# Kernel tuning notes

Measured on AMD Instinct MI355X. Metric: run time of the kernel, lower is better.

## Reference

```python
import jax, jax.numpy as jnp
import numpy as np

B, S, D = 1, 2048, 2048
H, KVH, HD = 32, 8, 64  # heads, kv heads, head_dim
GROUPS = H // KVH
SCALE = HD ** -0.5


def rotate_half(x):
    x1, x2 = jnp.split(x, 2, axis=-1)
    return jnp.concatenate((-x2, x1), axis=-1)


def setup_inputs() -> dict:
    key = jax.random.key(0)
    ks = jax.random.split(key, 8)
    hidden_states = jax.random.normal(ks[0], (B, S, D), dtype=jnp.float32)
    # RoPE tables: [B, S, HD]
    inv_freq = 1.0 / (10000.0 ** (jnp.arange(0, HD, 2, dtype=jnp.float32) / HD))
    t = jnp.arange(S, dtype=jnp.float32)
    freqs = jnp.outer(t, inv_freq)                      # [S, HD/2]
    emb = jnp.concatenate((freqs, freqs), axis=-1)      # [S, HD]
    cos = jnp.cos(emb)[None]                            # [1, S, HD]
    sin = jnp.sin(emb)[None]
    std = 0.02
    wq = jax.random.normal(ks[1], (H * HD, D), dtype=jnp.float32) * std
    wk = jax.random.normal(ks[2], (KVH * HD, D), dtype=jnp.float32) * std
    wv = jax.random.normal(ks[3], (KVH * HD, D), dtype=jnp.float32) * std
    wo = jax.random.normal(ks[4], (D, H * HD), dtype=jnp.float32) * std
    return {"hidden_states": hidden_states, "cos": cos, "sin": sin,
            "wq": wq, "wk": wk, "wv": wv, "wo": wo}


def reference(hidden_states, cos, sin, wq, wk, wv, wo):
    b, s, d = hidden_states.shape
    # QKV projections (nn.Linear: x @ W.T), split into heads -> [B, H, S, HD]
    q = (hidden_states @ wq.T).reshape(b, s, H, HD).transpose(0, 2, 1, 3)
    k = (hidden_states @ wk.T).reshape(b, s, KVH, HD).transpose(0, 2, 1, 3)
    v = (hidden_states @ wv.T).reshape(b, s, KVH, HD).transpose(0, 2, 1, 3)
    # RoPE (unsqueeze_dim=1)
    c = cos[:, None, :, :]
    sn = sin[:, None, :, :]
    q = q * c + rotate_half(q) * sn
    k = k * c + rotate_half(k) * sn
    # GQA: repeat kv heads to match query heads
    k = jnp.repeat(k, GROUPS, axis=1)
    v = jnp.repeat(v, GROUPS, axis=1)
    # scaled causal softmax attention
    scores = jnp.einsum('bhqd,bhkd->bhqk', q, k) * SCALE
    causal = jnp.tril(jnp.ones((s, s), dtype=bool))
    scores = jnp.where(causal, scores, jnp.finfo(scores.dtype).min)
    probs = jax.nn.softmax(scores, axis=-1)
    attn = jnp.einsum('bhqk,bhkd->bhqd', probs, v)
    attn = attn.transpose(0, 2, 1, 3).reshape(b, s, H * HD)
    return attn @ wo.T
```

## Files before the change

### kernel.cpp

```cpp
#include <hip/hip_runtime.h>
#include <stdint.h>

#define SEQ   2048
#define DMODEL 2048
#define NQH   32
#define NKVH  8
#define HDIM  64
#define QN    (NQH*HDIM)
#define KVNN  (NKVH*HDIM)

typedef __bf16 bf16x8 __attribute__((ext_vector_type(8)));
typedef float  f32x4  __attribute__((ext_vector_type(4)));
typedef unsigned short u16;

__device__ __forceinline__ u16 f2bf(float f) {
  uint32_t u = __builtin_bit_cast(uint32_t, f);
  u += 0x7fffu + ((u >> 16) & 1u);
  return (u16)(u >> 16);
}
__device__ __forceinline__ float bf2f(u16 b) {
  return __builtin_bit_cast(float, (uint32_t)b << 16);
}
__device__ __forceinline__ bool probe_is_f32(const uint32_t* p) {
  return (p[0] & 0xFFFFu) == 0u;
}

__device__ __forceinline__ void glds16(const u16* g, void* lds) {
  __builtin_amdgcn_global_load_lds(
      (const __attribute__((address_space(1))) uint32_t*)g,
      (__attribute__((address_space(3))) uint32_t*)lds, 16, 0, 0);
}

__global__ __launch_bounds__(256)
void conv_all(const void* __restrict__ X, const void* __restrict__ cosv,
              const void* __restrict__ sinv, const void* __restrict__ wq,
              const void* __restrict__ wk, const void* __restrict__ wv,
              const void* __restrict__ wo,
              u16* __restrict__ Xc, u16* __restrict__ cosc, u16* __restrict__ sinc,
              u16* __restrict__ wqc, u16* __restrict__ wkc, u16* __restrict__ wvc,
              u16* __restrict__ woc)
{
  const bool f32in = probe_is_f32((const uint32_t*)cosv);
  const long t = (long)blockIdx.x * 256 + threadIdx.x;
  const void* src; u16* dst; long off;
  if      (t < 524288L)  { src = X;    dst = Xc;   off = t; }
  else if (t < 1048576L) { src = wq;   dst = wqc;  off = t - 524288L; }
  else if (t < 1179648L) { src = wk;   dst = wkc;  off = t - 1048576L; }
  else if (t < 1310720L) { src = wv;   dst = wvc;  off = t - 1179648L; }
  else if (t < 1835008L) { src = wo;   dst = woc;  off = t - 1310720L; }
  else if (t < 1851392L) { src = cosv; dst = cosc; off = t - 1835008L; }
  else                   { src = sinv; dst = sinc; off = t - 1851392L; }
  if (f32in) {
    const float4* s = (const float4*)src;
    float4 a = s[2*off], b = s[2*off + 1];
    union { u16 h[8]; uint4 u; } o;
    o.h[0]=f2bf(a.x); o.h[1]=f2bf(a.y); o.h[2]=f2bf(a.z); o.h[3]=f2bf(a.w);
    o.h[4]=f2bf(b.x); o.h[5]=f2bf(b.y); o.h[6]=f2bf(b.z); o.h[7]=f2bf(b.w);
    *(uint4*)(dst + off*8) = o.u;
  } else {
    *(uint4*)(dst + off*8) = ((const uint4*)src)[off];
  }
}

__global__ __launch_bounds__(256, 4)
void gemm_qkv(const u16* __restrict__ A,
              const u16* __restrict__ wq, const u16* __restrict__ wk,
              const u16* __restrict__ wv,
              u16* __restrict__ Qb, u16* __restrict__ Kb, u16* __restrict__ Vb)
{
  __shared__ __align__(16) u16 As[64][32];
  __shared__ __align__(16) u16 Bs[128][32];
  const int tid  = threadIdx.x;
  const int wave = tid >> 6;
  const int lane = tid & 63;
  const int quad = lane >> 4;
  const int l16  = lane & 15;
  const int m0 = blockIdx.y * 64;
  const int n0 = blockIdx.x * 128;
  const int wm = (wave & 1) * 32;
  const int wn = (wave >> 1) * 64;
  const int K = DMODEL;
  const int lr = lane >> 2;
  const int lc = (lane & 3) * 8;

  const u16* Bbase; u16* Cbase; int Cstride, nc0;
  if (n0 < 2048)      { Bbase = wq + (size_t)n0 * K;          Cbase = Qb; Cstride = QN;   nc0 = n0; }
  else if (n0 < 2560) { Bbase = wk + (size_t)(n0 - 2048) * K; Cbase = Kb; Cstride = KVNN; nc0 = n0 - 2048; }
  else                { Bbase = wv + (size_t)(n0 - 2560) * K; Cbase = Vb; Cstride = KVNN; nc0 = n0 - 2560; }

  f32x4 acc[2][4];
  #pragma unroll
  for (int i = 0; i < 2; i++)
    #pragma unroll
    for (int j = 0; j < 4; j++)
      acc[i][j] = (f32x4){0.f, 0.f, 0.f, 0.f};

  for (int k0 = 0; k0 < K; k0 += 32) {
    __syncthreads();
    glds16(A + (size_t)(m0 + 16*wave + lr) * K + k0 + lc,
           (char*)&As[0][0] + wave*1024);
    glds16(Bbase + (size_t)(16*wave + lr) * K + k0 + lc,
           (char*)&Bs[0][0] + wave*1024);
    glds16(Bbase + (size_t)(64 + 16*wave + lr) * K + k0 + lc,
           (char*)&Bs[0][0] + (4+wave)*1024);
    __syncthreads();
    bf16x8 af[2], bfr[4];
    #pragma unroll
    for (int i = 0; i < 2; i++) af[i]  = *(const bf16x8*)&As[wm + i*16 + l16][quad*8];
    #pragma unroll
    for (int j = 0; j < 4; j++) bfr[j] = *(const bf16x8*)&Bs[wn + j*16 + l16][quad*8];
    #pragma unroll
    for (int i = 0; i < 2; i++)
      #pragma unroll
      for (int j = 0; j < 4; j++)
        acc[i][j] = __builtin_amdgcn_mfma_f32_16x16x32_bf16(af[i], bfr[j], acc[i][j], 0, 0, 0);
  }

  #pragma unroll
  for (int i = 0; i < 2; i++) {
    const int rb = m0 + wm + i*16 + quad*4;
    #pragma unroll
    for (int j = 0; j < 4; j++) {
      const int col = nc0 + wn + j*16 + l16;
      #pragma unroll
      for (int r = 0; r < 4; r++)
        Cbase[(size_t)(rb + r) * Cstride + col] = f2bf(acc[i][j][r]);
    }
  }
}

__global__ __launch_bounds__(256, 4)
void gemm_nt(const u16* __restrict__ A, const u16* __restrict__ B,
             void* __restrict__ C, int M, int N, int K,
             const uint32_t* outprobe)
{
  __shared__ __align__(16) u16 As[64][32];
  __shared__ __align__(16) u16 Bs[128][32];
  const int tid  = threadIdx.x;
  const int wave = tid >> 6;
  const int lane = tid & 63;
  const int quad = lane >> 4;
  const int l16  = lane & 15;
  const int m0 = blockIdx.y * 64;
  const int n0 = blockIdx.x * 128;
  const int wm = (wave & 1) * 32;
  const int wn = (wave >> 1) * 64;
  const int lr = lane >> 2;
  const int lc = (lane & 3) * 8;

  f32x4 acc[2][4];
  #pragma unroll
  for (int i = 0; i < 2; i++)
    #pragma unroll
    for (int j = 0; j < 4; j++)
      acc[i][j] = (f32x4){0.f, 0.f, 0.f, 0.f};

  for (int k0 = 0; k0 < K; k0 += 32) {
    __syncthreads();
    glds16(A + (size_t)(m0 + 16*wave + lr) * K + k0 + lc,
           (char*)&As[0][0] + wave*1024);
    glds16(B + (size_t)(n0 + 16*wave + lr) * K + k0 + lc,
           (char*)&Bs[0][0] + wave*1024);
    glds16(B + (size_t)(n0 + 64 + 16*wave + lr) * K + k0 + lc,
           (char*)&Bs[0][0] + (4+wave)*1024);
    __syncthreads();
    bf16x8 af[2], bfr[4];
    #pragma unroll
    for (int i = 0; i < 2; i++) af[i]  = *(const bf16x8*)&As[wm + i*16 + l16][quad*8];
    #pragma unroll
    for (int j = 0; j < 4; j++) bfr[j] = *(const bf16x8*)&Bs[wn + j*16 + l16][quad*8];
    #pragma unroll
    for (int i = 0; i < 2; i++)
      #pragma unroll
      for (int j = 0; j < 4; j++)
        acc[i][j] = __builtin_amdgcn_mfma_f32_16x16x32_bf16(af[i], bfr[j], acc[i][j], 0, 0, 0);
  }

  const bool f32out = (outprobe != nullptr) && probe_is_f32(outprobe);
  #pragma unroll
  for (int i = 0; i < 2; i++) {
    const int rb = m0 + wm + i*16 + quad*4;
    #pragma unroll
    for (int j = 0; j < 4; j++) {
      const int col = n0 + wn + j*16 + l16;
      if (f32out) {
        float* Cf = (float*)C;
        #pragma unroll
        for (int r = 0; r < 4; r++)
          Cf[(size_t)(rb + r) * N + col] = acc[i][j][r];
      } else {
        u16* Ch = (u16*)C;
        #pragma unroll
        for (int r = 0; r < 4; r++)
          Ch[(size_t)(rb + r) * N + col] = f2bf(acc[i][j][r]);
      }
    }
  }
}

__global__ void rope_k(u16* __restrict__ Kb,
                       const u16* __restrict__ cosb, const u16* __restrict__ sinb)
{
  const int idx = blockIdx.x * 256 + threadIdx.x;
  const int s = idx >> 8;
  const int rem = idx & 255;
  u16* base = Kb + (size_t)s * KVNN + (rem >> 5) * 64;
  const int d = rem & 31;
  const float x1 = bf2f(base[d]);
  const float x2 = bf2f(base[d + 32]);
  const float c  = bf2f(cosb[s * 64 + d]);
  const float sn = bf2f(sinb[s * 64 + d]);
  base[d]      = f2bf(x1 * c - x2 * sn);
  base[d + 32] = f2bf(x2 * c + x1 * sn);
}

__global__ __launch_bounds__(256)
void vtrans(const u16* __restrict__ Vb, u16* __restrict__ Vtg)
{
  __shared__ __align__(16) u16 T[64][72];
  const int tid = threadIdx.x;
  const int hkv = blockIdx.x & 7;
  const int s0  = (blockIdx.x >> 3) * 64;
  const int r = tid >> 3;
  const int c = (tid & 7) * 8;
  *(uint4*)&T[r][c]      = *(const uint4*)(Vb + (size_t)(s0 + r)      * KVNN + hkv*64 + c);
  *(uint4*)&T[r + 32][c] = *(const uint4*)(Vb + (size_t)(s0 + r + 32) * KVNN + hkv*64 + c);
  __syncthreads();
  #pragma unroll
  for (int dd = 0; dd < 64; dd += 32) {
    const int d = (tid >> 3) + dd;
    union { u16 h[8]; uint4 u; } o;
    #pragma unroll
    for (int j = 0; j < 8; j++) o.h[j] = T[c + j][d];
    *(uint4*)(Vtg + (size_t)(hkv*64 + d) * SEQ + s0 + c) = o.u;
  }
}

__device__ __forceinline__ float qmax16(float v) {
  v = fmaxf(v, __shfl_xor(v, 1)); v = fmaxf(v, __shfl_xor(v, 2));
  v = fmaxf(v, __shfl_xor(v, 4)); v = fmaxf(v, __shfl_xor(v, 8));
  return v;
}
__device__ __forceinline__ float qsum16(float v) {
  v += __shfl_xor(v, 1); v += __shfl_xor(v, 2);
  v += __shfl_xor(v, 4); v += __shfl_xor(v, 8);
  return v;
}

__global__ __launch_bounds__(256, 4)
void attn_kernel(const u16* __restrict__ Qb,
                 const u16* __restrict__ Kb,
                 const u16* __restrict__ Vtg,
                 u16* __restrict__ Ob,
                 const u16* __restrict__ cosb, const u16* __restrict__ sinb)
{
  __shared__ __align__(16) u16 Ks[64][72];
  __shared__ __align__(16) u16 Vt[64][72];
  __shared__ __align__(16) u16 Ps[4][16][72];

  const int tid  = threadIdx.x;
  const int wave = tid >> 6;
  const int lane = tid & 63;
  const int quad = lane >> 4;
  const int l16  = lane & 15;
  const int h    = blockIdx.x;
  const int qt   = 31 - blockIdx.y;
  const int hkv  = h >> 2;
  const int qrow0 = qt * 64 + wave * 16;
  const int ktmax = qt + 1;

  bf16x8 qf[2];
  {
    const int qrow = qrow0 + l16;
    const u16* qp = Qb + (size_t)qrow * QN + h*64 + quad*8;
    union { bf16x8 v; u16 h8[8]; } lo, hi, cv, sv, olo, ohi;
    lo.v = *(const bf16x8*)qp;
    hi.v = *(const bf16x8*)(qp + 32);
    cv.v = *(const bf16x8*)(cosb + qrow*64 + quad*8);
    sv.v = *(const bf16x8*)(sinb + qrow*64 + quad*8);
    #pragma unroll
    for (int j = 0; j < 8; j++) {
      const float x1 = bf2f(lo.h8[j]), x2 = bf2f(hi.h8[j]);
      const float c = bf2f(cv.h8[j]), sn = bf2f(sv.h8[j]);
      olo.h8[j] = f2bf((x1*c - x2*sn) * 0.125f);
      ohi.h8[j] = f2bf((x2*c + x1*sn) * 0.125f);
    }
    qf[0] = olo.v;
    qf[1] = ohi.v;
  }

  f32x4 oacc[4];
  #pragma unroll
  for (int nt = 0; nt < 4; nt++) oacc[nt] = (f32x4){0.f, 0.f, 0.f, 0.f};
  float m_run[4], l_run[4];
  #pragma unroll
  for (int r = 0; r < 4; r++) { m_run[r] = -1e30f; l_run[r] = 0.f; }

  const int sr = tid >> 3;
  const int sc = (tid & 7) * 8;

  uint4 k0, k1, v0, v1;
  {
    k0 = *(const uint4*)(Kb + (size_t)(sr)      * KVNN + hkv*64 + sc);
    k1 = *(const uint4*)(Kb + (size_t)(sr + 32) * KVNN + hkv*64 + sc);
    v0 = *(const uint4*)(Vtg + (size_t)(hkv*64 + sr)      * SEQ + sc);
    v1 = *(const uint4*)(Vtg + (size_t)(hkv*64 + sr + 32) * SEQ + sc);
  }

  for (int kt = 0; kt < ktmax; kt++) {
    const int kb = kt * 64;
    const bool diag = (kt == qt);

    __syncthreads();
    *(uint4*)&Ks[sr][sc]      = k0;
    *(uint4*)&Ks[sr + 32][sc] = k1;
    *(uint4*)&Vt[sr][sc]      = v0;
    *(uint4*)&Vt[sr + 32][sc] = v1;
    __syncthreads();

    if (kt + 1 < ktmax) {
      const int kn = kb + 64;
      k0 = *(const uint4*)(Kb + (size_t)(kn + sr)      * KVNN + hkv*64 + sc);
      k1 = *(const uint4*)(Kb + (size_t)(kn + sr + 32) * KVNN + hkv*64 + sc);
      v0 = *(const uint4*)(Vtg + (size_t)(hkv*64 + sr)      * SEQ + kn + sc);
      v1 = *(const uint4*)(Vtg + (size_t)(hkv*64 + sr + 32) * SEQ + kn + sc);
    }

    f32x4 sacc[4];
    #pragma unroll
    for (int nt = 0; nt < 4; nt++) sacc[nt] = (f32x4){0.f, 0.f, 0.f, 0.f};
    #pragma unroll
    for (int ks = 0; ks < 2; ks++)
      #pragma unroll
      for (int nt = 0; nt < 4; nt++)
        if (!diag || nt <= wave) {
          bf16x8 kf = *(const bf16x8*)&Ks[nt*16 + l16][ks*32 + quad*8];
          sacc[nt] = __builtin_amdgcn_mfma_f32_16x16x32_bf16(qf[ks], kf, sacc[nt], 0, 0, 0);
        }
    if (diag) {
      #pragma unroll
      for (int nt = 0; nt < 4; nt++)
        #pragma unroll
        for (int r = 0; r < 4; r++)
          if (kb + nt*16 + l16 > qrow0 + quad*4 + r)
            sacc[nt][r] = -1e30f;
    }
    float alpha[4];
    #pragma unroll
    for (int r = 0; r < 4; r++) {
      float mx = fmaxf(fmaxf(sacc[0][r], sacc[1][r]), fmaxf(sacc[2][r], sacc[3][r]));
      mx = qmax16(mx);
      const float mnew = fmaxf(m_run[r], mx);
      alpha[r] = __expf(m_run[r] - mnew);
      m_run[r] = mnew;
      float rs = 0.f;
      #pragma unroll
      for (int nt = 0; nt < 4; nt++) {
        const float p = __expf(sacc[nt][r] - mnew);
        rs += p;
        Ps[wave][quad*4 + r][nt*16 + l16] = f2bf(p);
      }
      rs = qsum16(rs);
      l_run[r] = l_run[r] * alpha[r] + rs;
    }
    #pragma unroll
    for (int nt = 0; nt < 4; nt++)
      #pragma unroll
      for (int r = 0; r < 4; r++)
        oacc[nt][r] *= alpha[r];
    asm volatile("" ::: "memory");
    #pragma unroll
    for (int ks = 0; ks < 2; ks++) {
      if (diag && wave < 2 && ks == 1) continue;
      bf16x8 pf = *(const bf16x8*)&Ps[wave][l16][ks*32 + quad*8];
      #pragma unroll
      for (int nt = 0; nt < 4; nt++) {
        bf16x8 vf = *(const bf16x8*)&Vt[nt*16 + l16][ks*32 + quad*8];
        oacc[nt] = __builtin_amdgcn_mfma_f32_16x16x32_bf16(pf, vf, oacc[nt], 0, 0, 0);
      }
    }
  }

  #pragma unroll
  for (int r = 0; r < 4; r++) {
    const float inv = 1.0f / l_run[r];
    const int qrow = qrow0 + quad*4 + r;
    #pragma unroll
    for (int nt = 0; nt < 4; nt++)
      Ob[(size_t)qrow * QN + h*64 + nt*16 + l16] = f2bf(oacc[nt][r] * inv);
  }
}

extern "C" void kernel_launch(void* const* d_in, const int* in_sizes, int n_in,
                              void* d_out, int out_size, void* d_ws, size_t ws_size,
                              hipStream_t stream) {
  const void* X    = d_in[0];
  const void* cosr = d_in[1];
  const void* sinr = d_in[2];
  const void* wq   = d_in[3];
  const void* wk   = d_in[4];
  const void* wv   = d_in[5];
  const void* wo   = d_in[6];

  char* ws = (char*)d_ws;
  const size_t MB = 1024u * 1024u;
  u16* Xc   = (u16*)(ws);
  u16* wqc  = (u16*)(ws + 8*MB);
  u16* wkc  = (u16*)(ws + 16*MB);
  u16* wvc  = (u16*)(ws + 18*MB);
  u16* woc  = (u16*)(ws + 20*MB);
  u16* cosc = (u16*)(ws + 28*MB);
  u16* sinc = (u16*)(ws + 28*MB + 256*1024);
  u16* Qb   = (u16*)(ws + 28*MB + 512*1024);
  u16* Kb   = (u16*)(ws + 36*MB + 512*1024);
  u16* Vb   = (u16*)(ws + 38*MB + 512*1024);
  u16* Vtg  = (u16*)(ws + 40*MB + 512*1024);
  u16* Ab   = wqc;

  dim3 blk(256);
  conv_all<<<dim3(7296), blk, 0, stream>>>(X, cosr, sinr, wq, wk, wv, wo,
                                           Xc, cosc, sinc, wqc, wkc, wvc, woc);
  gemm_qkv<<<dim3(24, 32), blk, 0, stream>>>(Xc, wqc, wkc, wvc, Qb, Kb, Vb);
  rope_k<<<dim3((SEQ*NKVH*32)/256), blk, 0, stream>>>(Kb, cosc, sinc);
  vtrans<<<dim3(256), blk, 0, stream>>>(Vb, Vtg);
  attn_kernel<<<dim3(NQH, SEQ/64), blk, 0, stream>>>(Qb, Kb, Vtg, Ab, cosc, sinc);
  gemm_nt<<<dim3(16, 32), blk, 0, stream>>>(Ab, woc, d_out, SEQ, DMODEL, DMODEL,
                                            (const uint32_t*)cosr);
}
```

Baseline: 258.4 us.

## Double-buffer LDS and enlarge GEMM tiles to 128x128 in QKV and output projections

Both projection GEMMs move from 64x128 to 128x128 block tiles, so each wave computes a 64x64 sub-tile with 16 MFMAs per k-step instead of 8. The LDS staging becomes double-buffered: the next k-slice is prefetched with global_load_lds while the current one is consumed, leaving one barrier per iteration instead of two. This is meant to raise arithmetic intensity and hide global load latency. In exchange the grids halve to 384 and 256 blocks, occupancy drops to 2 blocks per CU, and register pressure rises, which may leave the 256-CU device underfilled.

```diff
diff --git a/kernel.cpp b/kernel.cpp
--- a/kernel.cpp
+++ b/kernel.cpp
@@ -29,6 +29,9 @@
   __builtin_amdgcn_global_load_lds(
       (const __attribute__((address_space(1))) uint32_t*)g,
       (__attribute__((address_space(3))) uint32_t*)lds, 16, 0, 0);
+}
+__device__ __forceinline__ void drain_vm() {
+  asm volatile("s_waitcnt vmcnt(0)" ::: "memory");
 }
 
 __global__ __launch_bounds__(256)
@@ -62,22 +65,22 @@
   }
 }
 
-__global__ __launch_bounds__(256, 4)
+__global__ __launch_bounds__(256, 2)
 void gemm_qkv(const u16* __restrict__ A,
               const u16* __restrict__ wq, const u16* __restrict__ wk,
               const u16* __restrict__ wv,
               u16* __restrict__ Qb, u16* __restrict__ Kb, u16* __restrict__ Vb)
 {
-  __shared__ __align__(16) u16 As[64][32];
-  __shared__ __align__(16) u16 Bs[128][32];
+  __shared__ __align__(16) u16 As[2][128][32];
+  __shared__ __align__(16) u16 Bs[2][128][32];
   const int tid  = threadIdx.x;
   const int wave = tid >> 6;
   const int lane = tid & 63;
   const int quad = lane >> 4;
   const int l16  = lane & 15;
-  const int m0 = blockIdx.y * 64;
+  const int m0 = blockIdx.y * 128;
   const int n0 = blockIdx.x * 128;
-  const int wm = (wave & 1) * 32;
+  const int wm = (wave & 1) * 64;
   const int wn = (wave >> 1) * 64;
   const int K = DMODEL;
   const int lr = lane >> 2;
@@ -88,36 +91,49 @@
   else if (n0 < 2560) { Bbase = wk + (size_t)(n0 - 2048) * K; Cbase = Kb; Cstride = KVNN; nc0 = n0 - 2048; }
   else                { Bbase = wv + (size_t)(n0 - 2560) * K; Cbase = Vb; Cstride = KVNN; nc0 = n0 - 2560; }
 
-  f32x4 acc[2][4];
-  #pragma unroll
-  for (int i = 0; i < 2; i++)
+  f32x4 acc[4][4];
+  #pragma unroll
+  for (int i = 0; i < 4; i++)
     #pragma unroll
     for (int j = 0; j < 4; j++)
       acc[i][j] = (f32x4){0.f, 0.f, 0.f, 0.f};
 
+  #define STAGE_QKV(b, k0)                                                        \
+    do {                                                                          \
+      glds16(A + (size_t)(m0 + 32*wave + lr) * K + (k0) + lc,                     \
+             (char*)&As[b][0][0] + wave*2048);                                    \
+      glds16(A + (size_t)(m0 + 32*wave + 16 + lr) * K + (k0) + lc,                \
+             (char*)&As[b][0][0] + wave*2048 + 1024);                             \
+      glds16(Bbase + (size_t)(32*wave + lr) * K + (k0) + lc,                      \
+             (char*)&Bs[b][0][0] + wave*2048);                                    \
+      glds16(Bbase + (size_t)(32*wave + 16 + lr) * K + (k0) + lc,                 \
+             (char*)&Bs[b][0][0] + wave*2048 + 1024);                             \
+    } while (0)
+
+  STAGE_QKV(0, 0);
+  drain_vm();
+  __syncthreads();
+  int cur = 0;
   for (int k0 = 0; k0 < K; k0 += 32) {
-    __syncthreads();
-    glds16(A + (size_t)(m0 + 16*wave + lr) * K + k0 + lc,
-           (char*)&As[0][0] + wave*1024);
-    glds16(Bbase + (size_t)(16*wave + lr) * K + k0 + lc,
-           (char*)&Bs[0][0] + wave*1024);
-    glds16(Bbase + (size_t)(64 + 16*wave + lr) * K + k0 + lc,
-           (char*)&Bs[0][0] + (4+wave)*1024);
-    __syncthreads();
-    bf16x8 af[2], bfr[4];
-    #pragma unroll
-    for (int i = 0; i < 2; i++) af[i]  = *(const bf16x8*)&As[wm + i*16 + l16][quad*8];
-    #pragma unroll
-    for (int j = 0; j < 4; j++) bfr[j] = *(const bf16x8*)&Bs[wn + j*16 + l16][quad*8];
-    #pragma unroll
-    for (int i = 0; i < 2; i++)
+    if (k0 + 32 < K) STAGE_QKV(cur ^ 1, k0 + 32);
+    bf16x8 af[4], bfr[4];
+    #pragma unroll
+    for (int i = 0; i < 4; i++) af[i]  = *(const bf16x8*)&As[cur][wm + i*16 + l16][quad*8];
+    #pragma unroll
+    for (int j = 0; j < 4; j++) bfr[j] = *(const bf16x8*)&Bs[cur][wn + j*16 + l16][quad*8];
+    #pragma unroll
+    for (int i = 0; i < 4; i++)
       #pragma unroll
       for (int j = 0; j < 4; j++)
         acc[i][j] = __builtin_amdgcn_mfma_f32_16x16x32_bf16(af[i], bfr[j], acc[i][j], 0, 0, 0);
-  }
-
-  #pragma unroll
-  for (int i = 0; i < 2; i++) {
+    drain_vm();
+    __syncthreads();
+    cur ^= 1;
+  }
+  #undef STAGE_QKV
+
+  #pragma unroll
+  for (int i = 0; i < 4; i++) {
     const int rb = m0 + wm + i*16 + quad*4;
     #pragma unroll
     for (int j = 0; j < 4; j++) {
@@ -129,56 +145,69 @@
   }
 }
 
-__global__ __launch_bounds__(256, 4)
+__global__ __launch_bounds__(256, 2)
 void gemm_nt(const u16* __restrict__ A, const u16* __restrict__ B,
              void* __restrict__ C, int M, int N, int K,
              const uint32_t* outprobe)
 {
-  __shared__ __align__(16) u16 As[64][32];
-  __shared__ __align__(16) u16 Bs[128][32];
+  __shared__ __align__(16) u16 As[2][128][32];
+  __shared__ __align__(16) u16 Bs[2][128][32];
   const int tid  = threadIdx.x;
   const int wave = tid >> 6;
   const int lane = tid & 63;
   const int quad = lane >> 4;
   const int l16  = lane & 15;
-  const int m0 = blockIdx.y * 64;
+  const int m0 = blockIdx.y * 128;
   const int n0 = blockIdx.x * 128;
-  const int wm = (wave & 1) * 32;
+  const int wm = (wave & 1) * 64;
   const int wn = (wave >> 1) * 64;
   const int lr = lane >> 2;
   const int lc = (lane & 3) * 8;
 
-  f32x4 acc[2][4];
-  #pragma unroll
-  for (int i = 0; i < 2; i++)
+  f32x4 acc[4][4];
+  #pragma unroll
+  for (int i = 0; i < 4; i++)
     #pragma unroll
     for (int j = 0; j < 4; j++)
       acc[i][j] = (f32x4){0.f, 0.f, 0.f, 0.f};
 
+  #define STAGE_NT(b, k0)                                                         \
+    do {                                                                          \
+      glds16(A + (size_t)(m0 + 32*wave + lr) * K + (k0) + lc,                     \
+             (char*)&As[b][0][0] + wave*2048);                                    \
+      glds16(A + (size_t)(m0 + 32*wave + 16 + lr) * K + (k0) + lc,                \
+             (char*)&As[b][0][0] + wave*2048 + 1024);                             \
+      glds16(B + (size_t)(n0 + 32*wave + lr) * K + (k0) + lc,                     \
+             (char*)&Bs[b][0][0] + wave*2048);                                    \
+      glds16(B + (size_t)(n0 + 32*wave + 16 + lr) * K + (k0) + lc,                \
+             (char*)&Bs[b][0][0] + wave*2048 + 1024);                             \
+    } while (0)
+
+  STAGE_NT(0, 0);
+  drain_vm();
+  __syncthreads();
+  int cur = 0;
   for (int k0 = 0; k0 < K; k0 += 32) {
-    __syncthreads();
-    glds16(A + (size_t)(m0 + 16*wave + lr) * K + k0 + lc,
-           (char*)&As[0][0] + wave*1024);
-    glds16(B + (size_t)(n0 + 16*wave + lr) * K + k0 + lc,
-           (char*)&Bs[0][0] + wave*1024);
-    glds16(B + (size_t)(n0 + 64 + 16*wave + lr) * K + k0 + lc,
-           (char*)&Bs[0][0] + (4+wave)*1024);
-    __syncthreads();
-    bf16x8 af[2], bfr[4];
-    #pragma unroll
-    for (int i = 0; i < 2; i++) af[i]  = *(const bf16x8*)&As[wm + i*16 + l16][quad*8];
-    #pragma unroll
-    for (int j = 0; j < 4; j++) bfr[j] = *(const bf16x8*)&Bs[wn + j*16 + l16][quad*8];
-    #pragma unroll
-    for (int i = 0; i < 2; i++)
+    if (k0 + 32 < K) STAGE_NT(cur ^ 1, k0 + 32);
+    bf16x8 af[4], bfr[4];
+    #pragma unroll
+    for (int i = 0; i < 4; i++) af[i]  = *(const bf16x8*)&As[cur][wm + i*16 + l16][quad*8];
+    #pragma unroll
+    for (int j = 0; j < 4; j++) bfr[j] = *(const bf16x8*)&Bs[cur][wn + j*16 + l16][quad*8];
+    #pragma unroll
+    for (int i = 0; i < 4; i++)
       #pragma unroll
       for (int j = 0; j < 4; j++)
         acc[i][j] = __builtin_amdgcn_mfma_f32_16x16x32_bf16(af[i], bfr[j], acc[i][j], 0, 0, 0);
-  }
+    drain_vm();
+    __syncthreads();
+    cur ^= 1;
+  }
+  #undef STAGE_NT
 
   const bool f32out = (outprobe != nullptr) && probe_is_f32(outprobe);
   #pragma unroll
-  for (int i = 0; i < 2; i++) {
+  for (int i = 0; i < 4; i++) {
     const int rb = m0 + wm + i*16 + quad*4;
     #pragma unroll
     for (int j = 0; j < 4; j++) {
@@ -420,10 +449,10 @@
   dim3 blk(256);
   conv_all<<<dim3(7296), blk, 0, stream>>>(X, cosr, sinr, wq, wk, wv, wo,
                                            Xc, cosc, sinc, wqc, wkc, wvc, woc);
-  gemm_qkv<<<dim3(24, 32), blk, 0, stream>>>(Xc, wqc, wkc, wvc, Qb, Kb, Vb);
+  gemm_qkv<<<dim3(24, 16), blk, 0, stream>>>(Xc, wqc, wkc, wvc, Qb, Kb, Vb);
   rope_k<<<dim3((SEQ*NKVH*32)/256), blk, 0, stream>>>(Kb, cosc, sinc);
   vtrans<<<dim3(256), blk, 0, stream>>>(Vb, Vtg);
   attn_kernel<<<dim3(NQH, SEQ/64), blk, 0, stream>>>(Qb, Kb, Vtg, Ab, cosc, sinc);
-  gemm_nt<<<dim3(16, 32), blk, 0, stream>>>(Ab, woc, d_out, SEQ, DMODEL, DMODEL,
+  gemm_nt<<<dim3(16, 16), blk, 0, stream>>>(Ab, woc, d_out, SEQ, DMODEL, DMODEL,
                                             (const uint32_t*)cosr);
 }
```

After: 268.3 us. 3.8% more time.

## Double-buffer GEMM LDS tiles, use native bf16 conversion and exp2 softmax

Applied to the files above, without the earlier changes.

Both GEMM kernels get double-buffered LDS tiles. Each step prefetches the next K-slice with global_load_lds while computing MFMA on the current one, with one barrier per iteration instead of two. The attention softmax now scales scores by log2(e) and uses a hardware exp2 builtin instead of __expf, and f2bf uses the compiler's native bf16 conversion. Doubling LDS may reduce occupancy, and the full vmcnt(0) drain each iteration limits how much overlap is achieved.

```diff
diff --git a/kernel.cpp b/kernel.cpp
--- a/kernel.cpp
+++ b/kernel.cpp
@@ -14,12 +14,18 @@
 typedef unsigned short u16;
 
 __device__ __forceinline__ u16 f2bf(float f) {
-  uint32_t u = __builtin_bit_cast(uint32_t, f);
-  u += 0x7fffu + ((u >> 16) & 1u);
-  return (u16)(u >> 16);
+  __bf16 h = (__bf16)f;
+  return __builtin_bit_cast(u16, h);
 }
 __device__ __forceinline__ float bf2f(u16 b) {
   return __builtin_bit_cast(float, (uint32_t)b << 16);
+}
+__device__ __forceinline__ float fexp2(float x) {
+#if __has_builtin(__builtin_amdgcn_exp2f)
+  return __builtin_amdgcn_exp2f(x);
+#else
+  return __expf(0.69314718056f * x);
+#endif
 }
 __device__ __forceinline__ bool probe_is_f32(const uint32_t* p) {
   return (p[0] & 0xFFFFu) == 0u;
@@ -29,6 +35,9 @@
   __builtin_amdgcn_global_load_lds(
       (const __attribute__((address_space(1))) uint32_t*)g,
       (__attribute__((address_space(3))) uint32_t*)lds, 16, 0, 0);
+}
+__device__ __forceinline__ void drain_vm() {
+  asm volatile("s_waitcnt vmcnt(0)" ::: "memory");
 }
 
 __global__ __launch_bounds__(256)
@@ -68,8 +77,8 @@
               const u16* __restrict__ wv,
               u16* __restrict__ Qb, u16* __restrict__ Kb, u16* __restrict__ Vb)
 {
-  __shared__ __align__(16) u16 As[64][32];
-  __shared__ __align__(16) u16 Bs[128][32];
+  __shared__ __align__(16) u16 As[2][64][32];
+  __shared__ __align__(16) u16 Bs[2][128][32];
   const int tid  = threadIdx.x;
   const int wave = tid >> 6;
   const int lane = tid & 63;
@@ -95,26 +104,37 @@
     for (int j = 0; j < 4; j++)
       acc[i][j] = (f32x4){0.f, 0.f, 0.f, 0.f};
 
+  #define STAGE_QKV(b, k0)                                                        \
+    do {                                                                          \
+      glds16(A + (size_t)(m0 + 16*wave + lr) * K + (k0) + lc,                     \
+             (char*)&As[b][0][0] + wave*1024);                                    \
+      glds16(Bbase + (size_t)(16*wave + lr) * K + (k0) + lc,                      \
+             (char*)&Bs[b][0][0] + wave*1024);                                    \
+      glds16(Bbase + (size_t)(64 + 16*wave + lr) * K + (k0) + lc,                 \
+             (char*)&Bs[b][0][0] + (4+wave)*1024);                                \
+    } while (0)
+
+  STAGE_QKV(0, 0);
+  drain_vm();
+  __syncthreads();
+  int cur = 0;
   for (int k0 = 0; k0 < K; k0 += 32) {
-    __syncthreads();
-    glds16(A + (size_t)(m0 + 16*wave + lr) * K + k0 + lc,
-           (char*)&As[0][0] + wave*1024);
-    glds16(Bbase + (size_t)(16*wave + lr) * K + k0 + lc,
-           (char*)&Bs[0][0] + wave*1024);
-    glds16(Bbase + (size_t)(64 + 16*wave + lr) * K + k0 + lc,
-           (char*)&Bs[0][0] + (4+wave)*1024);
-    __syncthreads();
+    if (k0 + 32 < K) STAGE_QKV(cur ^ 1, k0 + 32);
     bf16x8 af[2], bfr[4];
     #pragma unroll
-    for (int i = 0; i < 2; i++) af[i]  = *(const bf16x8*)&As[wm + i*16 + l16][quad*8];
-    #pragma unroll
-    for (int j = 0; j < 4; j++) bfr[j] = *(const bf16x8*)&Bs[wn + j*16 + l16][quad*8];
+    for (int i = 0; i < 2; i++) af[i]  = *(const bf16x8*)&As[cur][wm + i*16 + l16][quad*8];
+    #pragma unroll
+    for (int j = 0; j < 4; j++) bfr[j] = *(const bf16x8*)&Bs[cur][wn + j*16 + l16][quad*8];
     #pragma unroll
     for (int i = 0; i < 2; i++)
       #pragma unroll
       for (int j = 0; j < 4; j++)
         acc[i][j] = __builtin_amdgcn_mfma_f32_16x16x32_bf16(af[i], bfr[j], acc[i][j], 0, 0, 0);
-  }
+    drain_vm();
+    __syncthreads();
+    cur ^= 1;
+  }
+  #undef STAGE_QKV
 
   #pragma unroll
   for (int i = 0; i < 2; i++) {
@@ -134,8 +154,8 @@
              void* __restrict__ C, int M, int N, int K,
              const uint32_t* outprobe)
 {
-  __shared__ __align__(16) u16 As[64][32];
-  __shared__ __align__(16) u16 Bs[128][32];
+  __shared__ __align__(16) u16 As[2][64][32];
+  __shared__ __align__(16) u16 Bs[2][128][32];
   const int tid  = threadIdx.x;
   const int wave = tid >> 6;
   const int lane = tid & 63;
@@ -155,26 +175,37 @@
     for (int j = 0; j < 4; j++)
       acc[i][j] = (f32x4){0.f, 0.f, 0.f, 0.f};
 
+  #define STAGE_NT(b, k0)                                                         \
+    do {                                                                          \
+      glds16(A + (size_t)(m0 + 16*wave + lr) * K + (k0) + lc,                     \
+             (char*)&As[b][0][0] + wave*1024);                                    \
+      glds16(B + (size_t)(n0 + 16*wave + lr) * K + (k0) + lc,                     \
+             (char*)&Bs[b][0][0] + wave*1024);                                    \
+      glds16(B + (size_t)(n0 + 64 + 16*wave + lr) * K + (k0) + lc,                \
+             (char*)&Bs[b][0][0] + (4+wave)*1024);                                \
+    } while (0)
+
+  STAGE_NT(0, 0);
+  drain_vm();
+  __syncthreads();
+  int cur = 0;
   for (int k0 = 0; k0 < K; k0 += 32) {
-    __syncthreads();
-    glds16(A + (size_t)(m0 + 16*wave + lr) * K + k0 + lc,
-           (char*)&As[0][0] + wave*1024);
-    glds16(B + (size_t)(n0 + 16*wave + lr) * K + k0 + lc,
-           (char*)&Bs[0][0] + wave*1024);
-    glds16(B + (size_t)(n0 + 64 + 16*wave + lr) * K + k0 + lc,
-           (char*)&Bs[0][0] + (4+wave)*1024);
-    __syncthreads();
+    if (k0 + 32 < K) STAGE_NT(cur ^ 1, k0 + 32);
     bf16x8 af[2], bfr[4];
     #pragma unroll
-    for (int i = 0; i < 2; i++) af[i]  = *(const bf16x8*)&As[wm + i*16 + l16][quad*8];
-    #pragma unroll
-    for (int j = 0; j < 4; j++) bfr[j] = *(const bf16x8*)&Bs[wn + j*16 + l16][quad*8];
+    for (int i = 0; i < 2; i++) af[i]  = *(const bf16x8*)&As[cur][wm + i*16 + l16][quad*8];
+    #pragma unroll
+    for (int j = 0; j < 4; j++) bfr[j] = *(const bf16x8*)&Bs[cur][wn + j*16 + l16][quad*8];
     #pragma unroll
     for (int i = 0; i < 2; i++)
       #pragma unroll
       for (int j = 0; j < 4; j++)
         acc[i][j] = __builtin_amdgcn_mfma_f32_16x16x32_bf16(af[i], bfr[j], acc[i][j], 0, 0, 0);
-  }
+    drain_vm();
+    __syncthreads();
+    cur ^= 1;
+  }
+  #undef STAGE_NT
 
   const bool f32out = (outprobe != nullptr) && probe_is_f32(outprobe);
   #pragma unroll
@@ -236,6 +267,8 @@
   }
 }
 
+#define LOG2E 1.4426950408889634f
+
 __device__ __forceinline__ float qmax16(float v) {
   v = fmaxf(v, __shfl_xor(v, 1)); v = fmaxf(v, __shfl_xor(v, 2));
   v = fmaxf(v, __shfl_xor(v, 4)); v = fmaxf(v, __shfl_xor(v, 8));
@@ -337,6 +370,11 @@
           bf16x8 kf = *(const bf16x8*)&Ks[nt*16 + l16][ks*32 + quad*8];
           sacc[nt] = __builtin_amdgcn_mfma_f32_16x16x32_bf16(qf[ks], kf, sacc[nt], 0, 0, 0);
         }
+    #pragma unroll
+    for (int nt = 0; nt < 4; nt++)
+      #pragma unroll
+      for (int r = 0; r < 4; r++)
+        sacc[nt][r] *= LOG2E;
     if (diag) {
       #pragma unroll
       for (int nt = 0; nt < 4; nt++)
@@ -351,12 +389,12 @@
       float mx = fmaxf(fmaxf(sacc[0][r], sacc[1][r]), fmaxf(sacc[2][r], sacc[3][r]));
       mx = qmax16(mx);
       const float mnew = fmaxf(m_run[r], mx);
-      alpha[r] = __expf(m_run[r] - mnew);
+      alpha[r] = fexp2(m_run[r] - mnew);
       m_run[r] = mnew;
       float rs = 0.f;
       #pragma unroll
       for (int nt = 0; nt < 4; nt++) {
-        const float p = __expf(sacc[nt][r] - mnew);
+        const float p = fexp2(sacc[nt][r] - mnew);
         rs += p;
         Ps[wave][quad*4 + r][nt*16 + l16] = f2bf(p);
       }
```

After: 250.7 us. -3.0%, faster.
